# Optimization experiments

Measured on AMD Instinct MI355X. Metric: run time of the kernel, lower is better.

The kernel has to match this reference:

```python
import jax, jax.numpy as jnp
from jax import lax
import numpy as np

B, T, L, D, TOPK, KC = 8, 4096, 256, 128, 8, 9  # KC = ctx conv kernel size


def setup_inputs() -> dict:
    key = jax.random.key(0)
    ks = jax.random.split(key, 9)
    s = 0.05
    return {
        "x": jax.random.normal(ks[0], (B, T), jnp.float32),
        "lag_embed": jax.random.normal(ks[1], (L + 1, D), jnp.float32) * s,  # nn.Embedding(L+1, d)
        "val_w": jax.random.normal(ks[2], (D, 1), jnp.float32) * s,          # nn.Linear(1, d) weight
        "val_b": jnp.zeros((D,), jnp.float32),
        "conv_w": jax.random.normal(ks[3], (D, 1, KC), jnp.float32) * s,     # Conv1d(1, d, 9) weight (O,I,K)
        "conv_b": jnp.zeros((D,), jnp.float32),
        "ctx_w": jax.random.normal(ks[4], (D, D), jnp.float32) * s,          # ctx_proj
        "ctx_b": jnp.zeros((D,), jnp.float32),
        "wq": jax.random.normal(ks[5], (D, D), jnp.float32) * s,             # Wq (no bias)
        "wk": jax.random.normal(ks[6], (D, D), jnp.float32) * s,             # Wk (no bias)
        "bias_w": jax.random.normal(ks[7], (1, D), jnp.float32) * s,         # bias_head
        "bias_b": jnp.zeros((1,), jnp.float32),
    }


def _lag_bank(x, Lv):
    # Xlags[b, t, l] = x[b, t-(l+1)], left-padded with zeros (per docstring/intended math)
    Bv, Tv = x.shape
    pads = jnp.pad(x, ((0, 0), (Lv, 0)))
    idx = Lv - 1 + jnp.arange(Tv)[:, None] - jnp.arange(Lv)[None, :]  # (T, L)
    return pads[:, idx]  # (B, T, L)


def reference(x, lag_embed, val_w, val_b, conv_w, conv_b, ctx_w, ctx_b, wq, wk, bias_w, bias_b):
    Xlags = _lag_bank(x, L)  # (B, T, L)

    # Causal context conv: left-pad 8 zeros, Conv1d(1, D, 9, padding=0)
    xp = jnp.pad(x, ((0, 0), (KC - 1, 0)))[:, None, :]  # (B, 1, T+8)
    ctx = lax.conv_general_dilated(xp, conv_w, (1,), 'VALID',
                                   dimension_numbers=('NCH', 'OIH', 'NCH'))
    ctx = ctx + conv_b[None, :, None]           # (B, D, T)
    ctx = jnp.transpose(ctx, (0, 2, 1))         # (B, T, D)
    ctx = ctx @ ctx_w.T + ctx_b                 # ctx_proj

    q = ctx @ wq.T                              # (B, T, D)
    # score = <q, Wk Hlag> = <Wk^T q, Hlag>; Hlag = Xlags*val_w + (val_b + lag_embed[1:L+1])
    # is rank-1 in the value -> never materialize the (B,T,L,D) tensor.
    qk = q @ wk                                 # (B, T, D) = Wk^T q
    base = val_b[None, :] + lag_embed[1:L + 1]  # (L, D)
    logits = Xlags * (qk @ val_w[:, 0])[:, :, None] + qk @ base.T  # (B, T, L)

    # top-k sparsification (ties are measure-zero with continuous inputs)
    kth = lax.top_k(logits, TOPK)[0][..., -1:]
    masked = jnp.where(logits >= kth, logits, -jnp.inf)
    w = jax.nn.softmax(masked, axis=-1)         # (B, T, L)

    mu = jnp.sum(w * Xlags, axis=-1) + (ctx @ bias_w.T)[..., 0] + bias_b[0]  # (B, T)
    return mu, w
```

## Files before the change

### kernel.cpp

```cpp
#include <hip/hip_runtime.h>
#include <math.h>

#define D   128
#define LQ  256
#define KCQ 9
#define BQ  8
#define TQ  4096
#define RISK_DELTA 2e-5f
#define WCAP 16384

__global__ void pk12(const float* __restrict__ wk, const float* __restrict__ wq,
                     const float* __restrict__ ctx_w, const float* __restrict__ bias_w,
                     const float* __restrict__ conv_w, const float* __restrict__ conv_b,
                     const float* __restrict__ ctx_b, const float* __restrict__ val_b,
                     const float* __restrict__ lag_embed,
                     double* __restrict__ u, int* __restrict__ wcnt,
                     double* __restrict__ g, double* __restrict__ c1,
                     float* __restrict__ ctx_wT, float* __restrict__ wqT,
                     float* __restrict__ conv_wT, float* __restrict__ baseT) {
    __shared__ double dT2[D];
    __shared__ double rowM[D];
    int tid = threadIdx.x;
    int bid = blockIdx.x;
    if (bid < D) {
        int d = bid;
        if (tid < D) {
            double acc = 0.0;
            for (int j = 0; j < D; ++j)
                acc += (double)wk[j * D + d] * (double)wq[j * D + tid];
            dT2[tid] = acc;
            ctx_wT[d * D + tid] = ctx_w[tid * D + d];
            wqT[d * D + tid]    = wq[tid * D + d];
            if (d < KCQ) conv_wT[d * D + tid] = conv_w[tid * KCQ + d];
        }
        baseT[d * LQ + tid] = __fadd_rn(val_b[d], lag_embed[(size_t)(tid + 1) * D + d]);
        __syncthreads();
        if (tid < D) {
            double acc = 0.0;
            for (int j = 0; j < D; ++j)
                acc += dT2[j] * (double)ctx_w[j * D + tid];
            rowM[tid] = acc;
        }
        __syncthreads();
        if (tid < KCQ) {
            double a = 0.0;
            for (int q = 0; q < D; ++q) a += rowM[q] * (double)conv_w[q * KCQ + tid];
            g[tid * D + d] = a;
        } else if (tid == KCQ) {
            double a = 0.0;
            for (int q = 0; q < D; ++q) a += rowM[q] * (double)conv_b[q];
            for (int q = 0; q < D; ++q) a += dT2[q] * (double)ctx_b[q];
            c1[d] = a;
        }
    } else if (bid == D) {
        if (tid < D) {
            double acc = 0.0;
            for (int dd = 0; dd < D; ++dd)
                acc += (double)bias_w[dd] * (double)ctx_w[dd * D + tid];
            u[tid] = acc;
        }
    } else {
        if (tid == 0) *wcnt = 0;
    }
}

__global__ void pk3(const float* __restrict__ lag_embed, const float* __restrict__ val_b,
                    const float* __restrict__ val_w, const float* __restrict__ conv_w,
                    const float* __restrict__ conv_b, const float* __restrict__ ctx_b,
                    const float* __restrict__ bias_w, const float* __restrict__ bias_b,
                    const double* __restrict__ g, const double* __restrict__ c1,
                    const double* __restrict__ u,
                    float* __restrict__ gbTf, float* __restrict__ cbvf, float* __restrict__ cstf) {
    int tid = threadIdx.x;
    if (blockIdx.x < LQ) {
        __shared__ double bl[D];
        int l = blockIdx.x;
        bl[tid] = (double)val_b[tid] + (double)lag_embed[(l + 1) * D + tid];
        __syncthreads();
        if (tid < KCQ) {
            double a = 0.0;
            for (int q = 0; q < D; ++q) a += bl[q] * g[tid * D + q];
            gbTf[tid * LQ + l] = (float)a;
        } else if (tid == KCQ) {
            double a = 0.0;
            for (int q = 0; q < D; ++q) a += bl[q] * c1[q];
            cbvf[l] = (float)a;
        }
    } else {
        if (tid < KCQ) {
            double a = 0.0, a2 = 0.0;
            for (int q = 0; q < D; ++q) a  += g[tid * D + q] * (double)val_w[q];
            for (int q = 0; q < D; ++q) a2 += u[q] * (double)conv_w[q * KCQ + tid];
            cstf[tid]      = (float)a;
            cstf[10 + tid] = (float)a2;
        } else if (tid == KCQ) {
            double a = 0.0, a2 = 0.0;
            for (int q = 0; q < D; ++q) a  += c1[q] * (double)val_w[q];
            for (int q = 0; q < D; ++q) a2 += u[q] * (double)conv_b[q];
            for (int q = 0; q < D; ++q) a2 += (double)bias_w[q] * (double)ctx_b[q];
            cstf[9]  = (float)a;
            cstf[19] = (float)(a2 + (double)bias_b[0]);
        }
    }
}

__global__ __launch_bounds__(256, 8) void lag_main(
    const float* __restrict__ x, const float* __restrict__ gbTf,
    const float* __restrict__ cbvf, const float* __restrict__ cstf,
    float* __restrict__ muOut, float* __restrict__ wOut,
    int* __restrict__ wcnt, int* __restrict__ wlist) {
    __shared__ float sgb[KCQ * LQ];
    __shared__ float scb[LQ];
    __shared__ float sc[20];
    int tid = threadIdx.x;
    #pragma unroll
    for (int i = 0; i < KCQ; ++i) sgb[i * LQ + tid] = gbTf[i * LQ + tid];
    scb[tid] = cbvf[tid];
    if (tid < 20) sc[tid] = cstf[tid];
    __syncthreads();

    int wave = tid >> 6, lane = tid & 63;
    int row = blockIdx.x * 4 + wave;
    int b = row >> 12;
    int t = row & (TQ - 1);
    const float* xb = x + b * TQ;

    float xw[KCQ];
    #pragma unroll
    for (int k = 0; k < KCQ; ++k) {
        int idx = t - 8 + k;
        xw[k] = (idx >= 0) ? xb[idx] : 0.f;
    }
    float s = sc[9], bias = sc[19];
    #pragma unroll
    for (int k = 0; k < KCQ; ++k) {
        s    = fmaf(sc[k],      xw[k], s);
        bias = fmaf(sc[10 + k], xw[k], bias);
    }

    int l0 = lane * 4;
    float xlag[4];
    #pragma unroll
    for (int i = 0; i < 4; ++i) {
        int idx = t - 1 - (l0 + i);
        xlag[i] = (idx >= 0) ? xb[idx] : 0.f;
    }

    float4 cb4 = *reinterpret_cast<const float4*>(&scb[l0]);
    float lg[4] = {cb4.x, cb4.y, cb4.z, cb4.w};
    #pragma unroll
    for (int k = 0; k < KCQ; ++k) {
        float4 g4 = *reinterpret_cast<const float4*>(&sgb[k * LQ + l0]);
        lg[0] = fmaf(g4.x, xw[k], lg[0]);
        lg[1] = fmaf(g4.y, xw[k], lg[1]);
        lg[2] = fmaf(g4.z, xw[k], lg[2]);
        lg[3] = fmaf(g4.w, xw[k], lg[3]);
    }
    #pragma unroll
    for (int i = 0; i < 4; ++i) lg[i] = fmaf(xlag[i], s, lg[i]);

    const float NEG_INF = -__builtin_inff();
    float wl0 = lg[0], wl1 = lg[1], wl2 = lg[2], wl3 = lg[3];
    float mx = 0.f, thr = 0.f, v9 = 0.f;
    #pragma unroll
    for (int it = 0; it < 9; ++it) {
        float lm = fmaxf(fmaxf(wl0, wl1), fmaxf(wl2, wl3));
        float m = lm;
        #pragma unroll
        for (int off = 32; off >= 1; off >>= 1)
            m = fmaxf(m, __shfl_xor(m, off, 64));
        if (it == 0) mx = m;
        if (it == 7) thr = m;
        if (it == 8) v9 = m;
        if (it < 8) {
            wl0 = (wl0 == m) ? NEG_INF : wl0;
            wl1 = (wl1 == m) ? NEG_INF : wl1;
            wl2 = (wl2 == m) ? NEG_INF : wl2;
            wl3 = (wl3 == m) ? NEG_INF : wl3;
        }
    }

    if ((thr - v9) < RISK_DELTA) {
        if (lane == 0) {
            int pos = atomicAdd(wcnt, 1);
            if (pos < WCAP) wlist[pos] = row;
        }
        return;
    }

    float p[4], psum = 0.f, pmu = 0.f;
    #pragma unroll
    for (int j = 0; j < 4; ++j) {
        p[j] = (lg[j] >= thr) ? __expf(lg[j] - mx) : 0.f;
        psum += p[j];
        pmu = fmaf(p[j], xlag[j], pmu);
    }
    #pragma unroll
    for (int off = 32; off >= 1; off >>= 1) {
        psum += __shfl_xor(psum, off, 64);
        pmu  += __shfl_xor(pmu,  off, 64);
    }
    float inv = 1.f / psum;
    float4 wo = make_float4(p[0] * inv, p[1] * inv, p[2] * inv, p[3] * inv);
    *reinterpret_cast<float4*>(&wOut[(size_t)row * LQ + l0]) = wo;
    if (lane == 0) muOut[row] = fmaf(pmu, inv, bias);
}

__global__ __launch_bounds__(512) void fixer(
    const float* __restrict__ x, const float* __restrict__ wk,
    const float* __restrict__ val_w, const float* __restrict__ conv_b,
    const float* __restrict__ ctx_b, const float* __restrict__ bias_w,
    const float* __restrict__ bias_b,
    const float* __restrict__ ctx_wT, const float* __restrict__ wqT,
    const float* __restrict__ conv_wT, const float* __restrict__ baseT,
    const int* __restrict__ wcnt, const int* __restrict__ wlist,
    float* __restrict__ muOut, float* __restrict__ wOut) {
    __shared__ float sxw[8][KCQ];
    __shared__ float sctxc[8][D];
    __shared__ float sctxp[8][D];
    __shared__ float sq[8][D];
    __shared__ float sqk[8][D];
    __shared__ float ssv[8];
    __shared__ float sbd[8];
    __shared__ float slog[8][LQ];
    __shared__ int   srow[8];

    int cnt = *wcnt;
    if (cnt > WCAP) cnt = WCAP;
    int ngroups = (cnt + 7) >> 3;
    int tid = threadIdx.x;

    for (int gi = blockIdx.x; gi < ngroups; gi += gridDim.x) {
        if (tid < 8) {
            int idx = gi * 8 + tid;
            if (idx >= cnt) idx = cnt - 1;
            srow[tid] = wlist[idx];
        }
        __syncthreads();
        if (tid < 8 * KCQ) {
            int g = tid / KCQ, k = tid % KCQ;
            int row = srow[g]; int b = row >> 12, t = row & (TQ - 1);
            int ii = t - 8 + k;
            sxw[g][k] = (ii >= 0) ? x[b * TQ + ii] : 0.f;
        }
        __syncthreads();

        {
            int d = tid & (D - 1), r = (tid >> 7) & 3;
            float cw[KCQ];
            #pragma unroll
            for (int k = 0; k < KCQ; ++k) cw[k] = conv_wT[k * D + d];
            float a0 = 0.f, a1 = 0.f;
            #pragma unroll
            for (int k = 0; k < KCQ; ++k) {
                a0 = fmaf(cw[k], sxw[r][k], a0);
                a1 = fmaf(cw[k], sxw[r + 4][k], a1);
            }
            float cb = conv_b[d];
            sctxc[r][d]     = __fadd_rn(a0, cb);
            sctxc[r + 4][d] = __fadd_rn(a1, cb);
        }
        __syncthreads();

        {
            int e = tid & (D - 1), r = (tid >> 7) & 3;
            float a0 = 0.f, a1 = 0.f;
            float wv0[16], wv1[16];
            #pragma unroll
            for (int u = 0; u < 16; ++u) wv0[u] = ctx_wT[u * D + e];
            #pragma unroll 1
            for (int d2 = 0; d2 < D; d2 += 32) {
                #pragma unroll
                for (int u = 0; u < 16; ++u) wv1[u] = ctx_wT[(d2 + 16 + u) * D + e];
                #pragma unroll
                for (int u = 0; u < 16; ++u) {
                    a0 = fmaf(wv0[u], sctxc[r][d2 + u], a0);
                    a1 = fmaf(wv0[u], sctxc[r + 4][d2 + u], a1);
                }
                if (d2 + 32 < D) {
                    #pragma unroll
                    for (int u = 0; u < 16; ++u) wv0[u] = ctx_wT[(d2 + 32 + u) * D + e];
                }
                #pragma unroll
                for (int u = 0; u < 16; ++u) {
                    a0 = fmaf(wv1[u], sctxc[r][d2 + 16 + u], a0);
                    a1 = fmaf(wv1[u], sctxc[r + 4][d2 + 16 + u], a1);
                }
            }
            float cb = ctx_b[e];
            sctxp[r][e]     = __fadd_rn(a0, cb);
            sctxp[r + 4][e] = __fadd_rn(a1, cb);
        }
        __syncthreads();

        {
            int e = tid & (D - 1), r = (tid >> 7) & 3;
            float a0 = 0.f, a1 = 0.f;
            float wv0[16], wv1[16];
            #pragma unroll
            for (int u = 0; u < 16; ++u) wv0[u] = wqT[u * D + e];
            #pragma unroll 1
            for (int e2 = 0; e2 < D; e2 += 32) {
                #pragma unroll
                for (int u = 0; u < 16; ++u) wv1[u] = wqT[(e2 + 16 + u) * D + e];
                #pragma unroll
                for (int u = 0; u < 16; ++u) {
                    a0 = fmaf(wv0[u], sctxp[r][e2 + u], a0);
                    a1 = fmaf(wv0[u], sctxp[r + 4][e2 + u], a1);
                }
                if (e2 + 32 < D) {
                    #pragma unroll
                    for (int u = 0; u < 16; ++u) wv0[u] = wqT[(e2 + 32 + u) * D + e];
                }
                #pragma unroll
                for (int u = 0; u < 16; ++u) {
                    a0 = fmaf(wv1[u], sctxp[r][e2 + 16 + u], a0);
                    a1 = fmaf(wv1[u], sctxp[r + 4][e2 + 16 + u], a1);
                }
            }
            sq[r][e]     = a0;
            sq[r + 4][e] = a1;
        }
        __syncthreads();

        {
            int e = tid & (D - 1), r = (tid >> 7) & 3;
            float a0 = 0.f, a1 = 0.f;
            float wv0[16], wv1[16];
            #pragma unroll
            for (int u = 0; u < 16; ++u) wv0[u] = wk[u * D + e];
            #pragma unroll 1
            for (int a2i = 0; a2i < D; a2i += 32) {
                #pragma unroll
                for (int u = 0; u < 16; ++u) wv1[u] = wk[(a2i + 16 + u) * D + e];
                #pragma unroll
                for (int u = 0; u < 16; ++u) {
                    a0 = fmaf(wv0[u], sq[r][a2i + u], a0);
                    a1 = fmaf(wv0[u], sq[r + 4][a2i + u], a1);
                }
                if (a2i + 32 < D) {
                    #pragma unroll
                    for (int u = 0; u < 16; ++u) wv0[u] = wk[(a2i + 32 + u) * D + e];
                }
                #pragma unroll
                for (int u = 0; u < 16; ++u) {
                    a0 = fmaf(wv1[u], sq[r][a2i + 16 + u], a0);
                    a1 = fmaf(wv1[u], sq[r + 4][a2i + 16 + u], a1);
                }
            }
            sqk[r][e]     = a0;
            sqk[r + 4][e] = a1;
        }
        __syncthreads();

        if (tid < 8) {
            int g = tid;
            float a = 0.f;
            #pragma unroll 1
            for (int d2 = 0; d2 < D; d2 += 16) {
                float vv[16];
                #pragma unroll
                for (int u = 0; u < 16; ++u) vv[u] = val_w[d2 + u];
                #pragma unroll
                for (int u = 0; u < 16; ++u) a = fmaf(sqk[g][d2 + u], vv[u], a);
            }
            ssv[g] = a;
        } else if (tid < 16) {
            int g = tid - 8;
            float a = 0.f;
            #pragma unroll 1
            for (int e2 = 0; e2 < D; e2 += 16) {
                float vv[16];
                #pragma unroll
                for (int u = 0; u < 16; ++u) vv[u] = bias_w[e2 + u];
                #pragma unroll
                for (int u = 0; u < 16; ++u) a = fmaf(sctxp[g][e2 + u], vv[u], a);
            }
            sbd[g] = a;
        }
        __syncthreads();

        {
            int l = tid & (LQ - 1);
            int h = tid >> 8;
            int r0 = h * 4;
            float c0 = 0.f, c1v = 0.f, c2 = 0.f, c3 = 0.f;
            float bd0[16], bd1[16];
            #pragma unroll
            for (int u = 0; u < 16; ++u) bd0[u] = baseT[u * LQ + l];
            #pragma unroll 1
            for (int d2 = 0; d2 < D; d2 += 32) {
                #pragma unroll
                for (int u = 0; u < 16; ++u) bd1[u] = baseT[(d2 + 16 + u) * LQ + l];
                #pragma unroll
                for (int u = 0; u < 16; ++u) {
                    float bd = bd0[u];
                    c0  = fmaf(bd, sqk[r0 + 0][d2 + u], c0);
                    c1v = fmaf(bd, sqk[r0 + 1][d2 + u], c1v);
                    c2  = fmaf(bd, sqk[r0 + 2][d2 + u], c2);
                    c3  = fmaf(bd, sqk[r0 + 3][d2 + u], c3);
                }
                if (d2 + 32 < D) {
                    #pragma unroll
                    for (int u = 0; u < 16; ++u) bd0[u] = baseT[(d2 + 32 + u) * LQ + l];
                }
                #pragma unroll
                for (int u = 0; u < 16; ++u) {
                    float bd = bd1[u];
                    c0  = fmaf(bd, sqk[r0 + 0][d2 + 16 + u], c0);
                    c1v = fmaf(bd, sqk[r0 + 1][d2 + 16 + u], c1v);
                    c2  = fmaf(bd, sqk[r0 + 2][d2 + 16 + u], c2);
                    c3  = fmaf(bd, sqk[r0 + 3][d2 + 16 + u], c3);
                }
            }
            float accs[4] = {c0, c1v, c2, c3};
            #pragma unroll
            for (int j = 0; j < 4; ++j) {
                int g = r0 + j;
                int row = srow[g]; int b = row >> 12, t = row & (TQ - 1);
                int ii = t - 1 - l;
                float xl = (ii >= 0) ? x[b * TQ + ii] : 0.f;
                slog[g][l] = __fadd_rn(__fmul_rn(xl, ssv[g]), accs[j]);
            }
        }
        __syncthreads();

        {
            int wv = tid >> 6, lane = tid & 63;
            int gg = wv;
            float lv0 = slog[gg][lane], lv1 = slog[gg][lane + 64];
            float lv2 = slog[gg][lane + 128], lv3 = slog[gg][lane + 192];
            const float NEG_INF = -__builtin_inff();
            float w0 = lv0, w1 = lv1, w2 = lv2, w3 = lv3;
            float mx = 0.f, thr = 0.f;
            #pragma unroll
            for (int it = 0; it < 8; ++it) {
                float lm = fmaxf(fmaxf(w0, w1), fmaxf(w2, w3));
                float m = lm;
                #pragma unroll
                for (int off = 32; off >= 1; off >>= 1)
                    m = fmaxf(m, __shfl_xor(m, off, 64));
                if (it == 0) mx = m;
                thr = m;
                if (it < 7) {
                    unsigned long long ball = __ballot(lm == m);
                    int leader = __ffsll(ball) - 1;
                    if (lane == leader) {
                        if (w0 == m)      w0 = NEG_INF;
                        else if (w1 == m) w1 = NEG_INF;
                        else if (w2 == m) w2 = NEG_INF;
                        else              w3 = NEG_INF;
                    }
                }
            }
            int row = srow[gg]; int b = row >> 12, t = row & (TQ - 1);
            float p[4], xlg[4];
            double ps = 0.0;
            float lvs[4] = {lv0, lv1, lv2, lv3};
            #pragma unroll
            for (int j = 0; j < 4; ++j) {
                int l = lane + 64 * j;
                int ii = t - 1 - l;
                xlg[j] = (ii >= 0) ? x[b * TQ + ii] : 0.f;
                p[j] = (lvs[j] >= thr) ? (float)exp((double)__fsub_rn(lvs[j], mx)) : 0.f;
                ps += (double)p[j];
            }
            #pragma unroll
            for (int off = 32; off >= 1; off >>= 1)
                ps += __shfl_xor(ps, off, 64);
            float psf = (float)ps;
            double mud = 0.0;
            #pragma unroll
            for (int j = 0; j < 4; ++j) {
                float wvv = __fdiv_rn(p[j], psf);
                wOut[(size_t)row * LQ + lane + 64 * j] = wvv;
                mud += (double)__fmul_rn(wvv, xlg[j]);
            }
            #pragma unroll
            for (int off = 32; off >= 1; off >>= 1)
                mud += __shfl_xor(mud, off, 64);
            if (lane == 0) {
                float m1 = (float)mud;
                m1 = __fadd_rn(m1, sbd[gg]);
                m1 = __fadd_rn(m1, bias_b[0]);
                muOut[row] = m1;
            }
        }
        __syncthreads();
    }
}

extern "C" void kernel_launch(void* const* d_in, const int* in_sizes, int n_in,
                              void* d_out, int out_size, void* d_ws, size_t ws_size,
                              hipStream_t stream) {
    const float* x         = (const float*)d_in[0];
    const float* lag_embed = (const float*)d_in[1];
    const float* val_w     = (const float*)d_in[2];
    const float* val_b     = (const float*)d_in[3];
    const float* conv_w    = (const float*)d_in[4];
    const float* conv_b    = (const float*)d_in[5];
    const float* ctx_w     = (const float*)d_in[6];
    const float* ctx_b     = (const float*)d_in[7];
    const float* wq        = (const float*)d_in[8];
    const float* wk        = (const float*)d_in[9];
    const float* bias_w    = (const float*)d_in[10];
    const float* bias_b    = (const float*)d_in[11];

    char* wsb = (char*)d_ws;
    double* T2  = (double*)wsb;
    double* g   = T2 + 16384;
    double* u   = g + 1152;
    double* c1  = u + 128;
    float* gbTf = (float*)(c1 + 128);
    float* cbvf = gbTf + 2304;
    float* cstf = cbvf + 256;
    int* wcnt  = (int*)(wsb + 163840);
    int* wlist = wcnt + 1;
    float* ctx_wT  = (float*)(wsb + 229504);
    float* wqT     = ctx_wT + 16384;
    float* conv_wT = wqT + 16384;
    float* baseT   = conv_wT + 1152;

    float* muOut = (float*)d_out;
    float* wOut  = muOut + BQ * TQ;

    hipLaunchKernelGGL(pk12, dim3(D + 2), dim3(256), 0, stream,
                       wk, wq, ctx_w, bias_w, conv_w, conv_b, ctx_b, val_b, lag_embed,
                       u, wcnt, g, c1, ctx_wT, wqT, conv_wT, baseT);
    hipLaunchKernelGGL(pk3, dim3(LQ + 1), dim3(D), 0, stream,
                       lag_embed, val_b, val_w, conv_w, conv_b, ctx_b, bias_w, bias_b,
                       g, c1, u, gbTf, cbvf, cstf);
    hipLaunchKernelGGL(lag_main, dim3(BQ * TQ / 4), dim3(256), 0, stream,
                       x, gbTf, cbvf, cstf, muOut, wOut, wcnt, wlist);
    hipLaunchKernelGGL(fixer, dim3(256), dim3(512), 0, stream,
                       x, wk, val_w, conv_b, ctx_b, bias_w, bias_b,
                       ctx_wT, wqT, conv_wT, baseT, wcnt, wlist, muOut, wOut);
}
```

Before: 89.96 us.

## Stage fixer weight matrices through a shared-memory buffer before each matvec

Adds a 64 KB shared buffer to the fixer kernel. Before each matvec stage it cooperatively copies the current weight matrix (ctx_wT, wqT, wk, then baseT in two halves) into that buffer with float4 loads, and the inner loops read weights from shared memory instead of strided global loads. The logits accumulation over D is split into two halves so each fits the buffer. It adds many extra block barriers and per-group reloads of the weights, and the large shared allocation lowers the number of blocks that can be resident per CU.

Result: slower. 98.25 us (+9.2%).

```diff
diff --git a/kernel.cpp b/kernel.cpp
--- a/kernel.cpp
+++ b/kernel.cpp
@@ -224,11 +224,19 @@
     __shared__ float sbd[8];
     __shared__ float slog[8][LQ];
     __shared__ int   srow[8];
+    __shared__ __align__(16) float swgt[D * D];
 
     int cnt = *wcnt;
     if (cnt > WCAP) cnt = WCAP;
     int ngroups = (cnt + 7) >> 3;
     int tid = threadIdx.x;
+
+    #define PRELOAD(src) do { \
+        const float4* s4 = reinterpret_cast<const float4*>(src); \
+        float4* d4 = reinterpret_cast<float4*>(swgt); \
+        _Pragma("unroll") \
+        for (int pk = 0; pk < 8; ++pk) d4[tid + pk * 512] = s4[tid + pk * 512]; \
+    } while (0)
 
     for (int gi = blockIdx.x; gi < ngroups; gi += gridDim.x) {
         if (tid < 8) {
@@ -245,6 +253,7 @@
         }
         __syncthreads();
 
+        PRELOAD(ctx_wT);
         {
             int d = tid & (D - 1), r = (tid >> 7) & 3;
             float cw[KCQ];
@@ -267,11 +276,11 @@
             float a0 = 0.f, a1 = 0.f;
             float wv0[16], wv1[16];
             #pragma unroll
-            for (int u = 0; u < 16; ++u) wv0[u] = ctx_wT[u * D + e];
+            for (int u = 0; u < 16; ++u) wv0[u] = swgt[u * D + e];
             #pragma unroll 1
             for (int d2 = 0; d2 < D; d2 += 32) {
                 #pragma unroll
-                for (int u = 0; u < 16; ++u) wv1[u] = ctx_wT[(d2 + 16 + u) * D + e];
+                for (int u = 0; u < 16; ++u) wv1[u] = swgt[(d2 + 16 + u) * D + e];
                 #pragma unroll
                 for (int u = 0; u < 16; ++u) {
                     a0 = fmaf(wv0[u], sctxc[r][d2 + u], a0);
@@ -279,7 +288,7 @@
                 }
                 if (d2 + 32 < D) {
                     #pragma unroll
-                    for (int u = 0; u < 16; ++u) wv0[u] = ctx_wT[(d2 + 32 + u) * D + e];
+                    for (int u = 0; u < 16; ++u) wv0[u] = swgt[(d2 + 32 + u) * D + e];
                 }
                 #pragma unroll
                 for (int u = 0; u < 16; ++u) {
@@ -292,17 +301,19 @@
             sctxp[r + 4][e] = __fadd_rn(a1, cb);
         }
         __syncthreads();
+        PRELOAD(wqT);
+        __syncthreads();
 
         {
             int e = tid & (D - 1), r = (tid >> 7) & 3;
             float a0 = 0.f, a1 = 0.f;
             float wv0[16], wv1[16];
             #pragma unroll
-            for (int u = 0; u < 16; ++u) wv0[u] = wqT[u * D + e];
+            for (int u = 0; u < 16; ++u) wv0[u] = swgt[u * D + e];
             #pragma unroll 1
             for (int e2 = 0; e2 < D; e2 += 32) {
                 #pragma unroll
-                for (int u = 0; u < 16; ++u) wv1[u] = wqT[(e2 + 16 + u) * D + e];
+                for (int u = 0; u < 16; ++u) wv1[u] = swgt[(e2 + 16 + u) * D + e];
                 #pragma unroll
                 for (int u = 0; u < 16; ++u) {
                     a0 = fmaf(wv0[u], sctxp[r][e2 + u], a0);
@@ -310,7 +321,7 @@
                 }
                 if (e2 + 32 < D) {
                     #pragma unroll
-                    for (int u = 0; u < 16; ++u) wv0[u] = wqT[(e2 + 32 + u) * D + e];
+                    for (int u = 0; u < 16; ++u) wv0[u] = swgt[(e2 + 32 + u) * D + e];
                 }
                 #pragma unroll
                 for (int u = 0; u < 16; ++u) {
@@ -321,6 +332,8 @@
             sq[r][e]     = a0;
             sq[r + 4][e] = a1;
         }
+        __syncthreads();
+        PRELOAD(wk);
         __syncthreads();
 
         {
@@ -328,11 +341,11 @@
             float a0 = 0.f, a1 = 0.f;
             float wv0[16], wv1[16];
             #pragma unroll
-            for (int u = 0; u < 16; ++u) wv0[u] = wk[u * D + e];
+            for (int u = 0; u < 16; ++u) wv0[u] = swgt[u * D + e];
             #pragma unroll 1
             for (int a2i = 0; a2i < D; a2i += 32) {
                 #pragma unroll
-                for (int u = 0; u < 16; ++u) wv1[u] = wk[(a2i + 16 + u) * D + e];
+                for (int u = 0; u < 16; ++u) wv1[u] = swgt[(a2i + 16 + u) * D + e];
                 #pragma unroll
                 for (int u = 0; u < 16; ++u) {
                     a0 = fmaf(wv0[u], sq[r][a2i + u], a0);
@@ -340,7 +353,7 @@
                 }
                 if (a2i + 32 < D) {
                     #pragma unroll
-                    for (int u = 0; u < 16; ++u) wv0[u] = wk[(a2i + 32 + u) * D + e];
+                    for (int u = 0; u < 16; ++u) wv0[u] = swgt[(a2i + 32 + u) * D + e];
                 }
                 #pragma unroll
                 for (int u = 0; u < 16; ++u) {
@@ -352,7 +365,7 @@
             sqk[r + 4][e] = a1;
         }
         __syncthreads();
-
+        PRELOAD(baseT);
         if (tid < 8) {
             int g = tid;
             float a = 0.f;
@@ -380,18 +393,19 @@
         }
         __syncthreads();
 
+        float c0, c1v, c2, c3;
         {
             int l = tid & (LQ - 1);
             int h = tid >> 8;
             int r0 = h * 4;
-            float c0 = 0.f, c1v = 0.f, c2 = 0.f, c3 = 0.f;
+            c0 = 0.f; c1v = 0.f; c2 = 0.f; c3 = 0.f;
             float bd0[16], bd1[16];
             #pragma unroll
-            for (int u = 0; u < 16; ++u) bd0[u] = baseT[u * LQ + l];
-            #pragma unroll 1
-            for (int d2 = 0; d2 < D; d2 += 32) {
-                #pragma unroll
-                for (int u = 0; u < 16; ++u) bd1[u] = baseT[(d2 + 16 + u) * LQ + l];
+            for (int u = 0; u < 16; ++u) bd0[u] = swgt[u * LQ + l];
+            #pragma unroll 1
+            for (int d2 = 0; d2 < 64; d2 += 32) {
+                #pragma unroll
+                for (int u = 0; u < 16; ++u) bd1[u] = swgt[(d2 + 16 + u) * LQ + l];
                 #pragma unroll
                 for (int u = 0; u < 16; ++u) {
                     float bd = bd0[u];
@@ -400,9 +414,46 @@
                     c2  = fmaf(bd, sqk[r0 + 2][d2 + u], c2);
                     c3  = fmaf(bd, sqk[r0 + 3][d2 + u], c3);
                 }
+                if (d2 + 32 < 64) {
+                    #pragma unroll
+                    for (int u = 0; u < 16; ++u) bd0[u] = swgt[(d2 + 32 + u) * LQ + l];
+                }
+                #pragma unroll
+                for (int u = 0; u < 16; ++u) {
+                    float bd = bd1[u];
+                    c0  = fmaf(bd, sqk[r0 + 0][d2 + 16 + u], c0);
+                    c1v = fmaf(bd, sqk[r0 + 1][d2 + 16 + u], c1v);
+                    c2  = fmaf(bd, sqk[r0 + 2][d2 + 16 + u], c2);
+                    c3  = fmaf(bd, sqk[r0 + 3][d2 + 16 + u], c3);
+                }
+            }
+        }
+        __syncthreads();
+        PRELOAD(baseT + 64 * LQ);
+        __syncthreads();
+
+        {
+            int l = tid & (LQ - 1);
+            int h = tid >> 8;
+            int r0 = h * 4;
+            float bd0[16], bd1[16];
+            #pragma unroll
+            for (int u = 0; u < 16; ++u) bd0[u] = swgt[u * LQ + l];
+            #pragma unroll 1
+            for (int d2 = 64; d2 < D; d2 += 32) {
+                #pragma unroll
+                for (int u = 0; u < 16; ++u) bd1[u] = swgt[(d2 - 64 + 16 + u) * LQ + l];
+                #pragma unroll
+                for (int u = 0; u < 16; ++u) {
+                    float bd = bd0[u];
+                    c0  = fmaf(bd, sqk[r0 + 0][d2 + u], c0);
+                    c1v = fmaf(bd, sqk[r0 + 1][d2 + u], c1v);
+                    c2  = fmaf(bd, sqk[r0 + 2][d2 + u], c2);
+                    c3  = fmaf(bd, sqk[r0 + 3][d2 + u], c3);
+                }
                 if (d2 + 32 < D) {
                     #pragma unroll
-                    for (int u = 0; u < 16; ++u) bd0[u] = baseT[(d2 + 32 + u) * LQ + l];
+                    for (int u = 0; u < 16; ++u) bd0[u] = swgt[(d2 - 64 + 32 + u) * LQ + l];
                 }
                 #pragma unroll
                 for (int u = 0; u < 16; ++u) {
@@ -488,6 +539,7 @@
         }
         __syncthreads();
     }
+    #undef PRELOAD
 }
 
 extern "C" void kernel_launch(void* const* d_in, const int* in_sizes, int n_in,
```
